# Kernel optimization log

Hardware: AMD Instinct MI355X
Metric: run time of the kernel (lower is better)

Reference implementation:

```python
import jax, jax.numpy as jnp
import numpy as np

B, N, T, D = 32, 19, 2048, 128
TOP_K = 3
THRESHOLD = 1e-4
TEMPERATURE = 0.1


def setup_inputs() -> dict:
    key = jax.random.key(0)
    features = jax.random.normal(key, (B, N, T, D), dtype=jnp.float32)
    return {"features": features}


def reference(features):
    b, n, t, d = features.shape
    # (B, N, T, D) -> (B*T, N, D)
    f = features.transpose(0, 2, 1, 3).reshape(b * t, n, d)
    # cosine similarity (F.normalize uses eps=1e-12 on the norm)
    norm = jnp.linalg.norm(f, axis=-1, keepdims=True)
    fn = f / jnp.maximum(norm, 1e-12)
    adj = jnp.einsum('bnd,bmd->bnm', fn, fn) / TEMPERATURE
    adj = jax.nn.softmax(adj, axis=-1)
    # top-k sparsification along last dim
    vals, idx = jax.lax.top_k(adj, TOP_K)
    adj = jnp.put_along_axis(jnp.zeros_like(adj), idx, vals, axis=-1, inplace=False)
    # threshold pruning
    adj = jnp.where(adj > THRESHOLD, adj, jnp.zeros_like(adj))
    # symmetrize
    adj = (adj + adj.transpose(0, 2, 1)) * 0.5
    return adj.reshape(b, t, n, n)
```

## Files before the change

kernel.cpp:

```cpp
#include <hip/hip_runtime.h>
#include <math.h>

namespace {

constexpr int kB = 32;
constexpr int kN = 19;
constexpr int kT = 2048;
constexpr int kD = 128;

constexpr int TILES = 6;
constexpr int TPT   = 10;
constexpr int BDIM  = 64;
constexpr int KC    = 16;
constexpr int SROW  = kN * KC;
constexpr int CHUNK_F4 = TILES * kN * (KC / 4);

constexpr int RPAD  = 21;
constexpr int TSTR  = 400;

constexpr int NT    = kB * kT;
constexpr int NGRID = (NT + TILES - 1) / TILES;

constexpr float kTempInv = 10.0f;
constexpr float kThresh  = 1e-4f;

__global__ __launch_bounds__(BDIM, 2)
void fused_graph_kernel(const float* __restrict__ feat, float* __restrict__ out)
{
    __shared__ float smem[TILES * TSTR + TILES * 20];

    const int lane = threadIdx.x;
    int tl = lane / TPT;
    const int sub = lane - tl * TPT;
    const bool laneValid = (tl < TILES);
    if (!laneValid) tl = TILES - 1;

    const int bi    = (sub >= 4) + (sub >= 7) + (sub >= 9);
    const int start = bi * 4 - (bi * (bi - 1)) / 2;
    const int bj    = bi + (sub - start);

    const int gt0 = blockIdx.x * TILES;
    const int vT  = (NT - gt0 < TILES) ? (NT - gt0) : TILES;

    int ar[5], bc[5];
#pragma unroll
    for (int r = 0; r < 5; ++r) { ar[r] = bi * 5 + r; if (ar[r] > kN - 1) ar[r] = kN - 1; }
#pragma unroll
    for (int c = 0; c < 5; ++c) { bc[c] = bj * 5 + c; if (bc[c] > kN - 1) bc[c] = kN - 1; }

    float acc[5][5];
#pragma unroll
    for (int r = 0; r < 5; ++r)
#pragma unroll
        for (int c = 0; c < 5; ++c) acc[r][c] = 0.f;

    for (int kc = 0; kc < kD; kc += KC) {
        for (int q = lane; q < CHUNK_F4; q += BDIM) {
            const int d4 = q & 3;
            const int r  = q >> 2;
            const int t  = r % TILES;
            const int n  = r / TILES;
            int g = gt0 + t;
            if (g > NT - 1) g = NT - 1;
            const size_t flat = (((size_t)(g >> 11) * kN + n) << 11) + (size_t)(g & (kT - 1));
            const float4 v = *(const float4*)(feat + (flat << 7) + kc + (d4 << 2));
            *(float4*)(&smem[t * SROW + n * KC + d4 * 4]) = v;
        }
        __syncthreads();

        const float* base = &smem[tl * SROW];
#pragma unroll
        for (int s0 = 0; s0 < 4; ++s0) {
            const int s = (s0 + sub) & 3;
            float4 ra[5], cb[5];
#pragma unroll
            for (int r = 0; r < 5; ++r)
                ra[r] = *(const float4*)(base + ar[r] * KC + s * 4);
            if (bi == bj) {
#pragma unroll
                for (int c = 0; c < 5; ++c) cb[c] = ra[c];
            } else {
#pragma unroll
                for (int c = 0; c < 5; ++c)
                    cb[c] = *(const float4*)(base + bc[c] * KC + s * 4);
            }
#pragma unroll
            for (int r = 0; r < 5; ++r)
#pragma unroll
                for (int c = 0; c < 5; ++c) {
                    acc[r][c] = fmaf(ra[r].x, cb[c].x, acc[r][c]);
                    acc[r][c] = fmaf(ra[r].y, cb[c].y, acc[r][c]);
                    acc[r][c] = fmaf(ra[r].z, cb[c].z, acc[r][c]);
                    acc[r][c] = fmaf(ra[r].w, cb[c].w, acc[r][c]);
                }
        }
        __syncthreads();
    }

    {
        float* g = &smem[tl * TSTR];
#pragma unroll
        for (int r = 0; r < 5; ++r) {
            const int i = bi * 5 + r;
#pragma unroll
            for (int c = 0; c < 5; ++c) {
                const int j = bj * 5 + c;
                if (laneValid && i < kN && j < kN) {
                    g[i * RPAD + j] = acc[r][c];
                    if (i != j) g[j * RPAD + i] = acc[r][c];
                }
            }
        }
    }
    __syncthreads();

    float* sInv = &smem[TILES * TSTR];
    for (int q = lane; q < TILES * kN; q += BDIM) {
        const int tt = q / kN;
        const int i  = q - tt * kN;
        const float nrm = sqrtf(smem[tt * TSTR + i * RPAD + i]);
        sInv[tt * 20 + i] = 1.0f / fmaxf(nrm, 1e-12f);
    }
    __syncthreads();

    for (int q = lane; q < TILES * kN; q += BDIM) {
        const int tt = q / kN;
        const int i  = q - tt * kN;
        float* row = &smem[tt * TSTR + i * RPAD];
        const float* invp = &sInv[tt * 20];
        const float si = invp[i] * kTempInv;

        float l[kN];
        float m = -3.0e38f;
#pragma unroll
        for (int j = 0; j < kN; ++j) {
            const float g = row[j] * si * invp[j];
            l[j] = g;
            m = fmaxf(m, g);
        }
        float ssum = 0.f;
#pragma unroll
        for (int j = 0; j < kN; ++j) {
            const float e = __expf(l[j] - m);
            l[j] = e;
            ssum += e;
        }
        const float rs = 1.0f / ssum;
#pragma unroll
        for (int j = 0; j < kN; ++j) l[j] *= rs;

        int k1 = 0; float v1 = -1.f;
#pragma unroll
        for (int j = 0; j < kN; ++j) if (l[j] > v1) { v1 = l[j]; k1 = j; }
        int k2 = -1; float v2 = -1.f;
#pragma unroll
        for (int j = 0; j < kN; ++j) if (j != k1 && l[j] > v2) { v2 = l[j]; k2 = j; }
        int k3 = -1; float v3 = -1.f;
#pragma unroll
        for (int j = 0; j < kN; ++j) if (j != k1 && j != k2 && l[j] > v3) { v3 = l[j]; k3 = j; }

#pragma unroll
        for (int j = 0; j < kN; ++j) {
            const float p = l[j];
            const bool keep = (j == k1 || j == k2 || j == k3) && (p > kThresh);
            row[j] = keep ? p : 0.f;
        }
    }
    __syncthreads();

    float* ob = out + (size_t)gt0 * (kN * kN);
    const int qMax = vT * (kN * kN);
    for (int q = lane; q < qMax; q += BDIM) {
        const int tt = q / (kN * kN);
        const int r  = q - tt * (kN * kN);
        const int i  = r / kN;
        const int j  = r - i * kN;
        const float v = 0.5f * (smem[tt * TSTR + i * RPAD + j] +
                                smem[tt * TSTR + j * RPAD + i]);
        ob[q] = v;
    }
}

}

extern "C" void kernel_launch(void* const* d_in, const int* in_sizes, int n_in,
                              void* d_out, int out_size, void* d_ws, size_t ws_size,
                              hipStream_t stream)
{
    const float* feat = (const float*)d_in[0];
    float* out = (float*)d_out;
    dim3 grid(NGRID);
    dim3 block(BDIM);
    hipLaunchKernelGGL(fused_graph_kernel, grid, block, 0, stream, feat, out);
}
```

Measured before the change: 977.5 us.

## Double-buffer feature chunks with async global-to-LDS loads

Replaces the synchronous global-load-then-LDS-store loop with direct global_load_lds DMA into two LDS stage buffers, so the next K-chunk loads while the current one is being computed. Global addresses are precomputed once per lane and advanced by a pointer bump. The LDS layout changes to n-major, tile-interleaved rows to match the DMA order. The __syncthreads per chunk is replaced by vmcnt waits, which is valid because the block is a single wavefront. This relies on exact waitcnt accounting (the lane<8 conditional issue may miscount) and reuses the stage buffer as the later scratch area.

```diff
diff --git a/kernel.cpp b/kernel.cpp
--- a/kernel.cpp
+++ b/kernel.cpp
@@ -12,8 +12,8 @@
 constexpr int TPT   = 10;
 constexpr int BDIM  = 64;
 constexpr int KC    = 16;
-constexpr int SROW  = kN * KC;
 constexpr int CHUNK_F4 = TILES * kN * (KC / 4);
+constexpr int STAGE_F4 = CHUNK_F4;
 
 constexpr int RPAD  = 21;
 constexpr int TSTR  = 400;
@@ -23,11 +23,32 @@
 
 constexpr float kTempInv = 10.0f;
 constexpr float kThresh  = 1e-4f;
+
+#define GLOAD16(GP, LP, OFF)                                            \
+    __builtin_amdgcn_global_load_lds(                                   \
+        (__attribute__((address_space(1))) void*)(GP),                  \
+        (__attribute__((address_space(3))) void*)(LP), 16, (OFF), 0)
+
+#define WAITV(N)                                                        \
+    do { asm volatile("s_waitcnt vmcnt(" #N ")" ::: "memory");          \
+         __builtin_amdgcn_sched_barrier(0); } while (0)
+
+template <int OFFB>
+__device__ __forceinline__ void issue_chunk(const float* const (&gsrc)[8],
+                                            float4* dst, int lane)
+{
+#pragma unroll
+    for (int i = 0; i < 7; ++i)
+        GLOAD16(gsrc[i], dst + i * 64, OFFB);
+    if (lane < 8)
+        GLOAD16(gsrc[7], dst + 7 * 64, OFFB);
+}
 
 __global__ __launch_bounds__(BDIM, 2)
 void fused_graph_kernel(const float* __restrict__ feat, float* __restrict__ out)
 {
-    __shared__ float smem[TILES * TSTR + TILES * 20];
+    __shared__ float4 stage[2][STAGE_F4];
+    float* smem = (float*)stage;
 
     const int lane = threadIdx.x;
     int tl = lane / TPT;
@@ -54,35 +75,36 @@
 #pragma unroll
         for (int c = 0; c < 5; ++c) acc[r][c] = 0.f;
 
-    for (int kc = 0; kc < kD; kc += KC) {
-        for (int q = lane; q < CHUNK_F4; q += BDIM) {
-            const int d4 = q & 3;
-            const int r  = q >> 2;
-            const int t  = r % TILES;
-            const int n  = r / TILES;
-            int g = gt0 + t;
-            if (g > NT - 1) g = NT - 1;
-            const size_t flat = (((size_t)(g >> 11) * kN + n) << 11) + (size_t)(g & (kT - 1));
-            const float4 v = *(const float4*)(feat + (flat << 7) + kc + (d4 << 2));
-            *(float4*)(&smem[t * SROW + n * KC + d4 * 4]) = v;
-        }
-        __syncthreads();
-
-        const float* base = &smem[tl * SROW];
+    const float* gsrc[8];
+#pragma unroll
+    for (int i = 0; i < 8; ++i) {
+        int q = i * 64 + lane;
+        if (q > CHUNK_F4 - 1) q = CHUNK_F4 - 1;
+        const int r  = q >> 2;
+        const int d4 = q & 3;
+        const int t  = r % TILES;
+        const int n  = r / TILES;
+        int g = gt0 + t;
+        if (g > NT - 1) g = NT - 1;
+        const size_t flat = (((size_t)(g >> 11) * kN + n) << 11) + (size_t)(g & (kT - 1));
+        gsrc[i] = feat + (flat << 7) + (d4 << 2);
+    }
+
+    auto compute = [&](const float4* sb) {
 #pragma unroll
         for (int s0 = 0; s0 < 4; ++s0) {
             const int s = (s0 + sub) & 3;
             float4 ra[5], cb[5];
 #pragma unroll
             for (int r = 0; r < 5; ++r)
-                ra[r] = *(const float4*)(base + ar[r] * KC + s * 4);
+                ra[r] = sb[(ar[r] * TILES + tl) * 4 + s];
             if (bi == bj) {
 #pragma unroll
                 for (int c = 0; c < 5; ++c) cb[c] = ra[c];
             } else {
 #pragma unroll
                 for (int c = 0; c < 5; ++c)
-                    cb[c] = *(const float4*)(base + bc[c] * KC + s * 4);
+                    cb[c] = sb[(bc[c] * TILES + tl) * 4 + s];
             }
 #pragma unroll
             for (int r = 0; r < 5; ++r)
@@ -94,8 +116,25 @@
                     acc[r][c] = fmaf(ra[r].w, cb[c].w, acc[r][c]);
                 }
         }
-        __syncthreads();
-    }
+    };
+
+    issue_chunk<0>(gsrc, stage[0], lane);
+    issue_chunk<64>(gsrc, stage[1], lane);
+    WAITV(8);
+    compute(stage[0]);
+#pragma unroll 1
+    for (int it = 0; it < 3; ++it) {
+#pragma unroll
+        for (int i = 0; i < 8; ++i) gsrc[i] += 32;
+        issue_chunk<0>(gsrc, stage[0], lane);
+        WAITV(8);
+        compute(stage[1]);
+        issue_chunk<64>(gsrc, stage[1], lane);
+        WAITV(8);
+        compute(stage[0]);
+    }
+    WAITV(0);
+    compute(stage[1]);
 
     {
         float* g = &smem[tl * TSTR];
```

After: 1.710 ms. 1.75x slower.
